# Optimization experiments

Measured on AMD Instinct MI355X. Metric: run time of the kernel, lower is better.

## Reference

```python
import jax, jax.numpy as jnp
import numpy as np

N = 50000   # nodes
E = 800000  # edges
D = 256     # in = hidden = out channels
R = 16      # num_relations (last index reserved for self-loops)
B = 8       # num_bases
LN_EPS = 1e-5


def setup_inputs() -> dict:
    key = jax.random.key(0)
    ks = jax.random.split(key, 20)
    s_basis = np.sqrt(2.0 / (D + D)).astype(np.float32)  # glorot-ish scale
    s_att = np.sqrt(2.0 / (R + B)).astype(np.float32)
    inp = {
        "x": jax.random.normal(ks[0], (N, D), dtype=jnp.float32),
        "edge_index": jax.random.randint(ks[1], (2, E), 0, N),
        "edge_type": jax.random.randint(ks[2], (E,), 0, R),
        "edge_attr": jax.random.uniform(ks[3], (E,), dtype=jnp.float32),
        # layer 1 params
        "basis1": jax.random.normal(ks[4], (B, D, D), dtype=jnp.float32) * s_basis,
        "att1": jax.random.normal(ks[5], (R, B), dtype=jnp.float32) * s_att,
        "root1": jax.random.normal(ks[6], (D, D), dtype=jnp.float32) * s_basis,
        "bias1": jnp.zeros((D,), dtype=jnp.float32),
        "ln1_g": jnp.ones((D,), dtype=jnp.float32),
        "ln1_b": jnp.zeros((D,), dtype=jnp.float32),
        # layer 2 params
        "basis2": jax.random.normal(ks[7], (B, D, D), dtype=jnp.float32) * s_basis,
        "att2": jax.random.normal(ks[8], (R, B), dtype=jnp.float32) * s_att,
        "root2": jax.random.normal(ks[9], (D, D), dtype=jnp.float32) * s_basis,
        "bias2": jnp.zeros((D,), dtype=jnp.float32),
        "ln2_g": jnp.ones((D,), dtype=jnp.float32),
        "ln2_b": jnp.zeros((D,), dtype=jnp.float32),
    }
    return inp


def _layer_norm(x, g, b):
    mu = jnp.mean(x, axis=-1, keepdims=True)
    var = jnp.mean(jnp.square(x - mu), axis=-1, keepdims=True)
    return (x - mu) * jax.lax.rsqrt(var + LN_EPS) * g + b


def _rgcn_layer(x, edge_index, edge_type, edge_attr, basis, att, root, bias):
    n = x.shape[0]
    r = att.shape[0]
    # W_r = sum_b a_rb V_b ; then per-relation transform of every node.
    weight = jnp.einsum('rb,bio->rio', att, basis)          # [R, D, D]
    H = jnp.einsum('ni,rio->nro', x, weight)                # [N, R, D]
    # append self-loops with relation index R-1 and confidence 1.0
    loop = jnp.arange(n, dtype=edge_index.dtype)
    src = jnp.concatenate([edge_index[0], loop])
    dst = jnp.concatenate([edge_index[1], loop])
    et = jnp.concatenate([edge_type, jnp.full((n,), r - 1, dtype=edge_type.dtype)])
    ea = jnp.concatenate([edge_attr, jnp.ones((n,), dtype=x.dtype)])
    msg = H[src, et] * ea[:, None]                          # [E+N, D]
    summ = jax.ops.segment_sum(msg, dst, num_segments=n)
    cnt = jax.ops.segment_sum(jnp.ones_like(ea), dst, num_segments=n)
    agg = summ / cnt[:, None]                               # scatter-mean (cnt >= 1 via self-loops)
    return agg + x @ root + bias


def reference(x, edge_index, edge_type, edge_attr,
              basis1, att1, root1, bias1, ln1_g, ln1_b,
              basis2, att2, root2, bias2, ln2_g, ln2_b):
    # input_proj / output_proj are Identity since in == hidden == out.
    h = x
    h_out = _rgcn_layer(h, edge_index, edge_type, edge_attr, basis1, att1, root1, bias1)
    h = jax.nn.relu(_layer_norm(h + h_out, ln1_g, ln1_b))
    h_out = _rgcn_layer(h, edge_index, edge_type, edge_attr, basis2, att2, root2, bias2)
    h = jax.nn.relu(_layer_norm(h + h_out, ln2_g, ln2_b))
    return h
```

## Files before the change

kernel.cpp:

```cpp
#include <hip/hip_runtime.h>
#include <stdint.h>

#define D 256
#define RREL 16
#define BB 8
#define K9 2304
#define LN_EPS 1e-5f
#define NT (K9 / 64)
#define BUFB 49152

typedef __attribute__((ext_vector_type(8))) short frag8;
typedef __attribute__((ext_vector_type(4))) float floatx4;
typedef __attribute__((ext_vector_type(2))) float float2v;
typedef __attribute__((ext_vector_type(2))) unsigned int uint2v;

__device__ __forceinline__ unsigned short f2bf(float f) {
    union { float f; uint32_t u; } v; v.f = f;
    uint32_t r = (v.u + 0x7FFFu + ((v.u >> 16) & 1u)) >> 16;
    return (unsigned short)r;
}
__device__ __forceinline__ float bf2f(unsigned short u) {
    union { uint32_t u; float f; } v; v.u = (uint32_t)u << 16;
    return v.f;
}
__device__ __forceinline__ float2v bfpair(uint32_t d) {
    union { uint32_t u; float f; } lo, hi;
    lo.u = d << 16; hi.u = d & 0xFFFF0000u;
    return (float2v){lo.f, hi.f};
}

__device__ __forceinline__ float2v pk_mul(float2v a, float2v b) {
    float2v d;
    asm("v_pk_mul_f32 %0, %1, %2" : "=v"(d) : "v"(a), "v"(b));
    return d;
}
__device__ __forceinline__ void pk_fma_lo(float2v& acc, float2v c, float2v x) {
    asm("v_pk_fma_f32 %0, %1, %2, %0 op_sel:[0,0,0] op_sel_hi:[1,0,1]"
        : "+v"(acc) : "v"(c), "v"(x));
}
__device__ __forceinline__ void pk_fma_hi(float2v& acc, float2v c, float2v x) {
    asm("v_pk_fma_f32 %0, %1, %2, %0 op_sel:[0,1,0] op_sel_hi:[1,1,1]"
        : "+v"(acc) : "v"(c), "v"(x));
}

__device__ __forceinline__ void gl2lds16(const unsigned short* g, char* l) {
    __builtin_amdgcn_global_load_lds((const __attribute__((address_space(1))) void*)g,
                                     (__attribute__((address_space(3))) void*)l, 16, 0, 0);
}

__device__ __forceinline__ void nt_store4(unsigned short* p, ushort4 v) {
    uint2v u;
    u.x = (uint32_t)v.x | ((uint32_t)v.y << 16);
    u.y = (uint32_t)v.z | ((uint32_t)v.w << 16);
    __builtin_nontemporal_store(u, (uint2v*)p);
}

__global__ __launch_bounds__(256) void k_cvt(const float* __restrict__ src,
                                             unsigned short* __restrict__ dst, int n4) {
    int i = blockIdx.x * 256 + threadIdx.x;
    if (i >= n4) return;
    float4 v = ((const float4*)src)[i];
    ushort4 o = make_ushort4(f2bf(v.x), f2bf(v.y), f2bf(v.z), f2bf(v.w));
    ((ushort4*)dst)[i] = o;
}

__global__ __launch_bounds__(256) void k_deg(const int* __restrict__ ei,
                                             int* __restrict__ deg, int E) {
    int t = blockIdx.x * 256 + threadIdx.x;
    int stride = gridDim.x * 256;
    int d[8];
#pragma unroll
    for (int j = 0; j < 8; ++j) {
        int e = t + j * stride;
        d[j] = (e < E) ? ei[E + e] : -1;
    }
#pragma unroll
    for (int j = 0; j < 8; ++j)
        if (d[j] >= 0) atomicAdd(&deg[d[j]], 1);
}

__global__ __launch_bounds__(256) void k_scan1(const int* __restrict__ deg,
                                               int* __restrict__ csum, int N) {
    __shared__ int sh[256];
    int n = blockIdx.x * 256 + threadIdx.x;
    sh[threadIdx.x] = (n < N) ? deg[n] : 0;
    __syncthreads();
    for (int off = 128; off > 0; off >>= 1) {
        if (threadIdx.x < off) sh[threadIdx.x] += sh[threadIdx.x + off];
        __syncthreads();
    }
    if (threadIdx.x == 0) csum[blockIdx.x] = sh[0];
}

__global__ __launch_bounds__(256) void k_scan3(const int* __restrict__ deg,
                                               const int* __restrict__ csum, int nch,
                                               int* __restrict__ rowptr,
                                               int* __restrict__ cursor,
                                               float* __restrict__ cnt, int N) {
    __shared__ int sh[256];
    int tid = threadIdx.x;
    int bid = blockIdx.x;
    int base;
    if (nch <= 256) {
        int c = (tid < nch) ? csum[tid] : 0;
        sh[tid] = c;
        __syncthreads();
        for (int off = 1; off < 256; off <<= 1) {
            int t = (tid >= off) ? sh[tid - off] : 0;
            __syncthreads();
            sh[tid] += t;
            __syncthreads();
        }
        base = sh[bid] - csum[bid];
        if (bid == 0 && tid == 255) rowptr[N] = sh[255];
        __syncthreads();
    } else {
        int s = 0;
        for (int i = 0; i < bid; ++i) s += csum[i];
        base = s;
        if (bid == 0 && tid == 0) {
            int tot = 0;
            for (int i = 0; i < nch; ++i) tot += csum[i];
            rowptr[N] = tot;
        }
    }
    int n = bid * 256 + tid;
    int v = (n < N) ? deg[n] : 0;
    sh[tid] = v;
    __syncthreads();
    for (int off = 1; off < 256; off <<= 1) {
        int t = (tid >= off) ? sh[tid - off] : 0;
        __syncthreads();
        sh[tid] += t;
        __syncthreads();
    }
    int excl = sh[tid] - v + base;
    if (n < N) {
        rowptr[n] = excl;
        cursor[n] = excl;
        cnt[n] = (float)(v + 1);
    }
}

__global__ __launch_bounds__(256) void k_scatter(const int* __restrict__ ei,
                                                 const int* __restrict__ et,
                                                 const float* __restrict__ ea,
                                                 int* __restrict__ cursor,
                                                 int2* __restrict__ ep, int E) {
    int t = blockIdx.x * 256 + threadIdx.x;
    int stride = gridDim.x * 256;
    int src[8], dst[8], typ[8]; float w[8]; bool v[8];
#pragma unroll
    for (int j = 0; j < 8; ++j) {
        int e = t + j * stride;
        v[j] = (e < E);
        if (v[j]) { src[j] = ei[e]; dst[j] = ei[E + e]; typ[j] = et[e]; w[j] = ea[e]; }
    }
    int p[8];
#pragma unroll
    for (int j = 0; j < 8; ++j)
        if (v[j]) p[j] = atomicAdd(&cursor[dst[j]], 1);
#pragma unroll
    for (int j = 0; j < 8; ++j)
        if (v[j]) ep[p[j]] = make_int2(src[j] | (typ[j] << 24), __float_as_int(w[j]));
}

__global__ __launch_bounds__(256) void k_prep_w(const float* __restrict__ basis,
                                                const float* __restrict__ root,
                                                unsigned short* __restrict__ Wt) {
    __shared__ float tile[64][65];
    int k0 = blockIdx.x * 64, o0 = blockIdx.y * 64;
    const float* src = (k0 < BB * D) ? (basis + (size_t)k0 * D)
                                     : (root + (size_t)(k0 - BB * D) * D);
    int tid = threadIdx.x;
#pragma unroll
    for (int t = 0; t < 16; ++t) {
        int idx = t * 256 + tid;
        int kk = idx >> 6, oo = idx & 63;
        tile[kk][oo] = src[(size_t)kk * D + o0 + oo];
    }
    __syncthreads();
#pragma unroll
    for (int t = 0; t < 16; ++t) {
        int idx = t * 256 + tid;
        int oo = idx >> 6, kk = idx & 63;
        Wt[(size_t)(o0 + oo) * K9 + k0 + kk] = f2bf(tile[kk][oo]);
    }
}

__device__ __forceinline__ void edge_fma(float2v g2[4][4], float2v c0, float2v c1,
                                         float2v c2, float2v c3,
                                         float2v x0, float2v x1) {
    pk_fma_lo(g2[0][0], c0, x0); pk_fma_lo(g2[1][0], c1, x0);
    pk_fma_lo(g2[2][0], c2, x0); pk_fma_lo(g2[3][0], c3, x0);
    pk_fma_hi(g2[0][1], c0, x0); pk_fma_hi(g2[1][1], c1, x0);
    pk_fma_hi(g2[2][1], c2, x0); pk_fma_hi(g2[3][1], c3, x0);
    pk_fma_lo(g2[0][2], c0, x1); pk_fma_lo(g2[1][2], c1, x1);
    pk_fma_lo(g2[2][2], c2, x1); pk_fma_lo(g2[3][2], c3, x1);
    pk_fma_hi(g2[0][3], c0, x1); pk_fma_hi(g2[1][3], c1, x1);
    pk_fma_hi(g2[3][3], c3, x1); pk_fma_hi(g2[2][3], c2, x1);
}

__device__ __forceinline__ void do_edge(float2v g2[4][4], const float* att_s,
                                        int2 pe, uint2 ud) {
    int r = (unsigned)pe.x >> 24;
    const float4* Ar = (const float4*)&att_s[r * BB];
    float4 a0 = Ar[0], a1 = Ar[1];
    float we = __int_as_float(pe.y);
    float2v w2 = {we, we};
    float2v c0 = pk_mul(w2, (float2v){a0.x, a0.y});
    float2v c1 = pk_mul(w2, (float2v){a0.z, a0.w});
    float2v c2 = pk_mul(w2, (float2v){a1.x, a1.y});
    float2v c3 = pk_mul(w2, (float2v){a1.z, a1.w});
    float2v x0 = bfpair(ud.x), x1 = bfpair(ud.y);
    edge_fma(g2, c0, c1, c2, c3, x0, x1);
}

__global__ __launch_bounds__(256) void k_gather(
    const unsigned short* __restrict__ xb, const float* __restrict__ att,
    const int* __restrict__ rowptr, const int2* __restrict__ ep,
    const float* __restrict__ cnt, unsigned short* __restrict__ G,
    int n0, int rows, int N) {
    __shared__ __align__(32) float att_s[RREL * BB];
    int tid = threadIdx.x;
    if (tid < RREL * BB) att_s[tid] = att[tid];
    __syncthreads();
    int wv = tid >> 6, lane = tid & 63;
    int rloc = blockIdx.x * 4 + wv;
    if (rloc >= rows) return;
    int n = n0 + rloc;
    unsigned short* gout = G + (size_t)rloc * K9 + lane * 4;
    if (n >= N) {
        ushort4 z = make_ushort4(0, 0, 0, 0);
#pragma unroll
        for (int b = 0; b <= BB; ++b) nt_store4(gout + b * D, z);
        return;
    }
    uint2 xu = *(const uint2*)&xb[(size_t)n * D + lane * 4];
    float2v xs0 = bfpair(xu.x), xs1 = bfpair(xu.y);
    float xv[4] = {xs0.x, xs0.y, xs1.x, xs1.y};

    float2v g2[4][4];
#pragma unroll
    for (int bp = 0; bp < 4; ++bp) {
        float2v ap = {att_s[(RREL - 1) * BB + 2 * bp],
                      att_s[(RREL - 1) * BB + 2 * bp + 1]};
#pragma unroll
        for (int j = 0; j < 4; ++j) {
            float2v xs = {xv[j], xv[j]};
            g2[bp][j] = ap * xs;
        }
    }

    int e0 = rowptr[n], e1 = rowptr[n + 1];
    int e = e0;
    for (; e + 4 <= e1; e += 4) {
        int2 pa = ep[e], pb = ep[e + 1], pc = ep[e + 2], pd = ep[e + 3];
        uint2 uA = *(const uint2*)&xb[(size_t)(pa.x & 0xFFFFFF) * D + lane * 4];
        uint2 uB = *(const uint2*)&xb[(size_t)(pb.x & 0xFFFFFF) * D + lane * 4];
        uint2 uC = *(const uint2*)&xb[(size_t)(pc.x & 0xFFFFFF) * D + lane * 4];
        uint2 uD = *(const uint2*)&xb[(size_t)(pd.x & 0xFFFFFF) * D + lane * 4];
        __builtin_amdgcn_sched_barrier(0);
        do_edge(g2, att_s, pa, uA);
        do_edge(g2, att_s, pb, uB);
        do_edge(g2, att_s, pc, uC);
        do_edge(g2, att_s, pd, uD);
    }
    if (e + 2 <= e1) {
        int2 pa = ep[e], pb = ep[e + 1];
        uint2 uA = *(const uint2*)&xb[(size_t)(pa.x & 0xFFFFFF) * D + lane * 4];
        uint2 uB = *(const uint2*)&xb[(size_t)(pb.x & 0xFFFFFF) * D + lane * 4];
        __builtin_amdgcn_sched_barrier(0);
        do_edge(g2, att_s, pa, uA);
        do_edge(g2, att_s, pb, uB);
        e += 2;
    }
    if (e < e1) {
        int2 pa = ep[e];
        uint2 uA = *(const uint2*)&xb[(size_t)(pa.x & 0xFFFFFF) * D + lane * 4];
        do_edge(g2, att_s, pa, uA);
    }
#pragma unroll
    for (int bp = 0; bp < 4; ++bp) {
        ushort4 o0 = make_ushort4(f2bf(g2[bp][0].x), f2bf(g2[bp][1].x),
                                  f2bf(g2[bp][2].x), f2bf(g2[bp][3].x));
        nt_store4(gout + (2 * bp) * D, o0);
        ushort4 o1 = make_ushort4(f2bf(g2[bp][0].y), f2bf(g2[bp][1].y),
                                  f2bf(g2[bp][2].y), f2bf(g2[bp][3].y));
        nt_store4(gout + (2 * bp + 1) * D, o1);
    }
    float cn = cnt[n];
    ushort4 o = make_ushort4(f2bf(cn * xv[0]), f2bf(cn * xv[1]),
                             f2bf(cn * xv[2]), f2bf(cn * xv[3]));
    nt_store4(gout + BB * D, o);
}

__global__ __launch_bounds__(1024, 4) void k_gemm(
    const unsigned short* __restrict__ G, const unsigned short* __restrict__ Wt,
    const float* __restrict__ hin, const float* __restrict__ cnt,
    const float* __restrict__ bias, const float* __restrict__ gln,
    const float* __restrict__ bln, float* __restrict__ hout,
    unsigned short* __restrict__ houtb, int n0, int N) {
    __shared__ __align__(16) char smem[2 * BUFB];
    float* ps   = (float*)smem;
    float* pq   = ps + 512;
    float* mu_s = ps + 1024;
    float* rs_s = ps + 1152;

    int tid = threadIdx.x;
    int wv = tid >> 6, lane = tid & 63;
    int quad = lane >> 4, l16 = lane & 15;
    int wm = wv >> 2, wn = wv & 3;
    int grow = blockIdx.x * 128;
    int nb = n0 + grow;

    int arow_s = tid >> 3, aslot_s = tid & 7;
    const unsigned short* gA =
        G + (size_t)(grow + arow_s) * K9 + ((aslot_s ^ (arow_s & 7)) << 3);
    char* lA = smem + (tid << 4);
    const unsigned short* gB[2]; char* lB[2];
#pragma unroll
    for (int t = 0; t < 2; ++t) {
        int c = t * 1024 + tid;
        int brow = c >> 3, bslot = c & 7;
        gB[t] = Wt + (size_t)brow * K9 + ((bslot ^ (brow & 7)) << 3);
        lB[t] = smem + 16384 + (c << 4);
    }

    floatx4 acc[2][4];
#pragma unroll
    for (int mf = 0; mf < 2; ++mf)
#pragma unroll
        for (int nf = 0; nf < 4; ++nf) acc[mf][nf] = (floatx4){0.f, 0.f, 0.f, 0.f};

    auto STAGE = [&](int it, int soff) {
        int koff = it * 64;
        gl2lds16(gA + koff, lA + soff);
        gl2lds16(gB[0] + koff, lB[0] + soff);
        gl2lds16(gB[1] + koff, lB[1] + soff);
    };
    auto COMPUTE = [&](int soff) {
        const char* Ab = smem + soff;
        const char* Bb = Ab + 16384;
#pragma unroll
        for (int kc = 0; kc < 2; ++kc) {
            int g = kc * 4 + quad;
            frag8 a[2], b[4];
#pragma unroll
            for (int mf = 0; mf < 2; ++mf) {
                int arow = wm * 32 + mf * 16 + l16;
                a[mf] = *(const frag8*)(Ab + arow * 128 + ((g ^ (arow & 7)) << 4));
            }
#pragma unroll
            for (int nf = 0; nf < 4; ++nf) {
                int brow = wn * 64 + nf * 16 + l16;
                b[nf] = *(const frag8*)(Bb + brow * 128 + ((g ^ (brow & 7)) << 4));
            }
#pragma unroll
            for (int mf = 0; mf < 2; ++mf)
#pragma unroll
                for (int nf = 0; nf < 4; ++nf)
                    acc[mf][nf] = __builtin_amdgcn_mfma_f32_16x16x32_bf16(
                        a[mf], b[nf], acc[mf][nf], 0, 0, 0);
        }
    };

    STAGE(0, 0);
    __syncthreads();
    for (int it = 0; it < NT; it += 2) {
        STAGE(it + 1, BUFB);
        COMPUTE(0);
        __syncthreads();
        if (it + 2 < NT) STAGE(it + 2, 0);
        COMPUTE(BUFB);
        __syncthreads();
    }

    int col[4]; float bic[4];
#pragma unroll
    for (int nf = 0; nf < 4; ++nf) {
        col[nf] = wn * 64 + nf * 16 + l16;
        bic[nf] = bias[col[nf]];
    }
#pragma unroll
    for (int mf = 0; mf < 2; ++mf) {
#pragma unroll
        for (int r = 0; r < 4; ++r) {
            int row = wm * 32 + mf * 16 + quad * 4 + r;
            int n = nb + row;
            float s = 0.f, sq = 0.f;
            if (n < N) {
                float inv = 1.0f / cnt[n];
                const float* hp = hin + (size_t)n * D;
#pragma unroll
                for (int nf = 0; nf < 4; ++nf) {
                    float v = acc[mf][nf][r] * inv + hp[col[nf]] + bic[nf];
                    acc[mf][nf][r] = v;
                    s += v; sq += v * v;
                }
            }
            s += __shfl_xor(s, 1); sq += __shfl_xor(sq, 1);
            s += __shfl_xor(s, 2); sq += __shfl_xor(sq, 2);
            s += __shfl_xor(s, 4); sq += __shfl_xor(sq, 4);
            s += __shfl_xor(s, 8); sq += __shfl_xor(sq, 8);
            if (l16 == 0) {
                ps[row * 4 + wn] = s;
                pq[row * 4 + wn] = sq;
            }
        }
    }
    __syncthreads();
    if (tid < 128) {
        float s  = ps[tid * 4] + ps[tid * 4 + 1] + ps[tid * 4 + 2] + ps[tid * 4 + 3];
        float sq = pq[tid * 4] + pq[tid * 4 + 1] + pq[tid * 4 + 2] + pq[tid * 4 + 3];
        float mu = s * (1.f / D);
        mu_s[tid] = mu;
        rs_s[tid] = rsqrtf(sq * (1.f / D) - mu * mu + LN_EPS);
    }
    __syncthreads();

    float gc[4], bc[4];
#pragma unroll
    for (int nf = 0; nf < 4; ++nf) {
        gc[nf] = gln[col[nf]];
        bc[nf] = bln[col[nf]];
    }
#pragma unroll
    for (int mf = 0; mf < 2; ++mf) {
#pragma unroll
        for (int r = 0; r < 4; ++r) {
            int row = wm * 32 + mf * 16 + quad * 4 + r;
            int n = nb + row;
            if (n >= N) continue;
            float mu = mu_s[row], rs = rs_s[row];
            float* op = hout + (size_t)n * D;
#pragma unroll
            for (int nf = 0; nf < 4; ++nf) {
                float o = fmaxf((acc[mf][nf][r] - mu) * rs * gc[nf] + bc[nf], 0.f);
                op[col[nf]] = o;
                if (houtb) houtb[(size_t)n * D + col[nf]] = f2bf(o);
            }
        }
    }
}

extern "C" void kernel_launch(void* const* d_in, const int* in_sizes, int n_in,
                              void* d_out, int out_size, void* d_ws, size_t ws_size,
                              hipStream_t stream) {
    const float* x      = (const float*)d_in[0];
    const int*   ei     = (const int*)d_in[1];
    const int*   et     = (const int*)d_in[2];
    const float* ea     = (const float*)d_in[3];
    const float* basis1 = (const float*)d_in[4];
    const float* att1   = (const float*)d_in[5];
    const float* root1  = (const float*)d_in[6];
    const float* bias1  = (const float*)d_in[7];
    const float* g1     = (const float*)d_in[8];
    const float* b1     = (const float*)d_in[9];
    const float* basis2 = (const float*)d_in[10];
    const float* att2   = (const float*)d_in[11];
    const float* root2  = (const float*)d_in[12];
    const float* bias2  = (const float*)d_in[13];
    const float* g2     = (const float*)d_in[14];
    const float* b2     = (const float*)d_in[15];
    float* out = (float*)d_out;

    int N = in_sizes[0] / D;
    int E = in_sizes[2];
    int nch = (N + 255) / 256;
    int Mp = ((N + 63) / 64) * 64;
    int T = Mp / 64;
    int Tpad = (T + 1) & ~1;

    char* p = (char*)d_ws;
    size_t used = 0;
    auto alloc = [&](size_t bytes) {
        char* q = p;
        size_t a = (bytes + 255) & ~(size_t)255;
        p += a; used += a;
        return q;
    };
    float*          h1     = (float*)alloc((size_t)N * D * 4);
    unsigned short* xb     = (unsigned short*)alloc((size_t)N * D * 2);
    unsigned short* h1b    = (unsigned short*)alloc((size_t)N * D * 2);
    unsigned short* Wt     = (unsigned short*)alloc((size_t)K9 * D * 2);
    int*            deg    = (int*)alloc((size_t)N * 4);
    int*            rowptr = (int*)alloc((size_t)(N + 1) * 4);
    int*            cursor = (int*)alloc((size_t)N * 4);
    float*          cnt    = (float*)alloc((size_t)N * 4);
    int2*           ep     = (int2*)alloc((size_t)E * 8);
    int*            csum   = (int*)alloc((size_t)nch * 4);
    size_t remain = (ws_size > used + 256) ? (ws_size - used - 256) : 0;
    size_t tile_bytes = (size_t)64 * K9 * 2;
    int ct_max = (int)(remain / tile_bytes);
    if (ct_max < 2) ct_max = 2;
    if (ct_max > Tpad) ct_max = Tpad;
    unsigned short* G = (unsigned short*)alloc((size_t)ct_max * tile_bytes);

    int nch2 = (Tpad + ct_max - 1) / ct_max;
    int ct = (Tpad + nch2 - 1) / nch2;
    ct = (ct + 1) & ~1;
    if (ct > ct_max) ct = ct_max & ~1;
    if (ct < 2) ct = 2;

    hipMemsetAsync(deg, 0, (size_t)N * 4, stream);
    int gE8 = (E + 2047) / 2048;
    k_deg<<<gE8, 256, 0, stream>>>(ei, deg, E);
    k_scan1<<<nch, 256, 0, stream>>>(deg, csum, N);
    k_scan3<<<nch, 256, 0, stream>>>(deg, csum, nch, rowptr, cursor, cnt, N);
    k_scatter<<<gE8, 256, 0, stream>>>(ei, et, ea, cursor, ep, E);
    k_cvt<<<(N * D / 4 + 255) / 256, 256, 0, stream>>>(x, xb, N * D / 4);

    const float* bas[2]  = {basis1, basis2};
    const float* attp[2] = {att1, att2};
    const float* rt[2]   = {root1, root2};
    const float* bi[2]   = {bias1, bias2};
    const float* lg[2]   = {g1, g2};
    const float* lb[2]   = {b1, b2};
    const unsigned short* gin[2] = {xb, h1b};
    const float* hres[2] = {x, h1};
    float*          hof[2] = {h1, out};
    unsigned short* hob[2] = {h1b, nullptr};

    for (int L = 0; L < 2; ++L) {
        k_prep_w<<<dim3(K9 / 64, D / 64), 256, 0, stream>>>(bas[L], rt[L], Wt);
        for (int c0 = 0; c0 < Tpad; c0 += ct) {
            int tiles = (Tpad - c0 < ct) ? (Tpad - c0) : ct;
            int rows = tiles * 64;
            int n0 = c0 * 64;
            k_gather<<<rows / 4, 256, 0, stream>>>(gin[L], attp[L], rowptr, ep,
                                                   cnt, G, n0, rows, N);
            k_gemm<<<rows / 128, 1024, 0, stream>>>(G, Wt, hres[L], cnt, bi[L],
                                                    lg[L], lb[L], hof[L], hob[L],
                                                    n0, N);
        }
    }
}
```

Before: 675.4 us.

## Read root-term activations directly in GEMM instead of staging them in G

The gather kernel no longer writes the cnt-scaled self features as a ninth K-slice of the G buffer, so G shrinks from 2304 to 2048 columns. The GEMM streams the last K-chunk straight from the bf16 node features into a separate accumulator that is added without the 1/cnt scaling. This cuts gather write traffic and G read traffic. The G stores also switch from nontemporal to ordinary stores. In exchange the GEMM holds a second accumulator set, which adds register pressure, and padded rows may read past the end of the feature array.

```diff
diff --git a/kernel.cpp b/kernel.cpp
--- a/kernel.cpp
+++ b/kernel.cpp
@@ -5,6 +5,7 @@
 #define RREL 16
 #define BB 8
 #define K9 2304
+#define KG 2048
 #define LN_EPS 1e-5f
 #define NT (K9 / 64)
 #define BUFB 49152
@@ -12,7 +13,6 @@
 typedef __attribute__((ext_vector_type(8))) short frag8;
 typedef __attribute__((ext_vector_type(4))) float floatx4;
 typedef __attribute__((ext_vector_type(2))) float float2v;
-typedef __attribute__((ext_vector_type(2))) unsigned int uint2v;
 
 __device__ __forceinline__ unsigned short f2bf(float f) {
     union { float f; uint32_t u; } v; v.f = f;
@@ -46,13 +46,6 @@
 __device__ __forceinline__ void gl2lds16(const unsigned short* g, char* l) {
     __builtin_amdgcn_global_load_lds((const __attribute__((address_space(1))) void*)g,
                                      (__attribute__((address_space(3))) void*)l, 16, 0, 0);
-}
-
-__device__ __forceinline__ void nt_store4(unsigned short* p, ushort4 v) {
-    uint2v u;
-    u.x = (uint32_t)v.x | ((uint32_t)v.y << 16);
-    u.y = (uint32_t)v.z | ((uint32_t)v.w << 16);
-    __builtin_nontemporal_store(u, (uint2v*)p);
 }
 
 __global__ __launch_bounds__(256) void k_cvt(const float* __restrict__ src,
@@ -198,7 +191,7 @@
     pk_fma_lo(g2[0][2], c0, x1); pk_fma_lo(g2[1][2], c1, x1);
     pk_fma_lo(g2[2][2], c2, x1); pk_fma_lo(g2[3][2], c3, x1);
     pk_fma_hi(g2[0][3], c0, x1); pk_fma_hi(g2[1][3], c1, x1);
-    pk_fma_hi(g2[3][3], c3, x1); pk_fma_hi(g2[2][3], c2, x1);
+    pk_fma_hi(g2[2][3], c2, x1); pk_fma_hi(g2[3][3], c3, x1);
 }
 
 __device__ __forceinline__ void do_edge(float2v g2[4][4], const float* att_s,
@@ -219,8 +212,7 @@
 __global__ __launch_bounds__(256) void k_gather(
     const unsigned short* __restrict__ xb, const float* __restrict__ att,
     const int* __restrict__ rowptr, const int2* __restrict__ ep,
-    const float* __restrict__ cnt, unsigned short* __restrict__ G,
-    int n0, int rows, int N) {
+    unsigned short* __restrict__ G, int n0, int rows, int N) {
     __shared__ __align__(32) float att_s[RREL * BB];
     int tid = threadIdx.x;
     if (tid < RREL * BB) att_s[tid] = att[tid];
@@ -229,11 +221,11 @@
     int rloc = blockIdx.x * 4 + wv;
     if (rloc >= rows) return;
     int n = n0 + rloc;
-    unsigned short* gout = G + (size_t)rloc * K9 + lane * 4;
+    unsigned short* gout = G + (size_t)rloc * KG + lane * 4;
     if (n >= N) {
         ushort4 z = make_ushort4(0, 0, 0, 0);
 #pragma unroll
-        for (int b = 0; b <= BB; ++b) nt_store4(gout + b * D, z);
+        for (int b = 0; b < BB; ++b) *(ushort4*)(gout + b * D) = z;
         return;
     }
     uint2 xu = *(const uint2*)&xb[(size_t)n * D + lane * 4];
@@ -284,19 +276,16 @@
     for (int bp = 0; bp < 4; ++bp) {
         ushort4 o0 = make_ushort4(f2bf(g2[bp][0].x), f2bf(g2[bp][1].x),
                                   f2bf(g2[bp][2].x), f2bf(g2[bp][3].x));
-        nt_store4(gout + (2 * bp) * D, o0);
+        *(ushort4*)(gout + (2 * bp) * D) = o0;
         ushort4 o1 = make_ushort4(f2bf(g2[bp][0].y), f2bf(g2[bp][1].y),
                                   f2bf(g2[bp][2].y), f2bf(g2[bp][3].y));
-        nt_store4(gout + (2 * bp + 1) * D, o1);
-    }
-    float cn = cnt[n];
-    ushort4 o = make_ushort4(f2bf(cn * xv[0]), f2bf(cn * xv[1]),
-                             f2bf(cn * xv[2]), f2bf(cn * xv[3]));
-    nt_store4(gout + BB * D, o);
+        *(ushort4*)(gout + (2 * bp + 1) * D) = o1;
+    }
 }
 
 __global__ __launch_bounds__(1024, 4) void k_gemm(
-    const unsigned short* __restrict__ G, const unsigned short* __restrict__ Wt,
+    const unsigned short* __restrict__ G, const unsigned short* __restrict__ xb,
+    const unsigned short* __restrict__ Wt,
     const float* __restrict__ hin, const float* __restrict__ cnt,
     const float* __restrict__ bias, const float* __restrict__ gln,
     const float* __restrict__ bln, float* __restrict__ hout,
@@ -315,8 +304,9 @@
     int nb = n0 + grow;
 
     int arow_s = tid >> 3, aslot_s = tid & 7;
-    const unsigned short* gA =
-        G + (size_t)(grow + arow_s) * K9 + ((aslot_s ^ (arow_s & 7)) << 3);
+    int swzA = (aslot_s ^ (arow_s & 7)) << 3;
+    const unsigned short* gAG = G + (size_t)(grow + arow_s) * KG + swzA;
+    const unsigned short* gAX = xb + (size_t)(nb + arow_s) * D + swzA;
     char* lA = smem + (tid << 4);
     const unsigned short* gB[2]; char* lB[2];
 #pragma unroll
@@ -328,18 +318,24 @@
     }
 
     floatx4 acc[2][4];
+    floatx4 acc2[2][4];
 #pragma unroll
     for (int mf = 0; mf < 2; ++mf)
 #pragma unroll
-        for (int nf = 0; nf < 4; ++nf) acc[mf][nf] = (floatx4){0.f, 0.f, 0.f, 0.f};
+        for (int nf = 0; nf < 4; ++nf) {
+            acc[mf][nf]  = (floatx4){0.f, 0.f, 0.f, 0.f};
+            acc2[mf][nf] = (floatx4){0.f, 0.f, 0.f, 0.f};
+        }
 
     auto STAGE = [&](int it, int soff) {
+        const unsigned short* sa =
+            (it < 32) ? (gAG + it * 64) : (gAX + (it - 32) * 64);
+        gl2lds16(sa, lA + soff);
         int koff = it * 64;
-        gl2lds16(gA + koff, lA + soff);
         gl2lds16(gB[0] + koff, lB[0] + soff);
         gl2lds16(gB[1] + koff, lB[1] + soff);
     };
-    auto COMPUTE = [&](int soff) {
+    auto COMPUTE = [&](int soff, floatx4 (&ac)[2][4]) {
         const char* Ab = smem + soff;
         const char* Bb = Ab + 16384;
 #pragma unroll
@@ -360,19 +356,27 @@
             for (int mf = 0; mf < 2; ++mf)
 #pragma unroll
                 for (int nf = 0; nf < 4; ++nf)
-                    acc[mf][nf] = __builtin_amdgcn_mfma_f32_16x16x32_bf16(
-                        a[mf], b[nf], acc[mf][nf], 0, 0, 0);
+                    ac[mf][nf] = __builtin_amdgcn_mfma_f32_16x16x32_bf16(
+                        a[mf], b[nf], ac[mf][nf], 0, 0, 0);
         }
     };
 
     STAGE(0, 0);
     __syncthreads();
-    for (int it = 0; it < NT; it += 2) {
+    for (int it = 0; it < 32; it += 2) {
         STAGE(it + 1, BUFB);
-        COMPUTE(0);
+        COMPUTE(0, acc);
+        __syncthreads();
+        STAGE(it + 2, 0);
+        COMPUTE(BUFB, acc);
+        __syncthreads();
+    }
+    for (int it = 32; it < NT; it += 2) {
+        STAGE(it + 1, BUFB);
+        COMPUTE(0, acc2);
         __syncthreads();
         if (it + 2 < NT) STAGE(it + 2, 0);
-        COMPUTE(BUFB);
+        COMPUTE(BUFB, acc2);
         __syncthreads();
     }
 
@@ -394,7 +398,8 @@
                 const float* hp = hin + (size_t)n * D;
 #pragma unroll
                 for (int nf = 0; nf < 4; ++nf) {
-                    float v = acc[mf][nf][r] * inv + hp[col[nf]] + bic[nf];
+                    float v = acc[mf][nf][r] * inv + acc2[mf][nf][r]
+                            + hp[col[nf]] + bic[nf];
                     acc[mf][nf][r] = v;
                     s += v; sq += v * v;
                 }
@@ -491,7 +496,7 @@
     int2*           ep     = (int2*)alloc((size_t)E * 8);
     int*            csum   = (int*)alloc((size_t)nch * 4);
     size_t remain = (ws_size > used + 256) ? (ws_size - used - 256) : 0;
-    size_t tile_bytes = (size_t)64 * K9 * 2;
+    size_t tile_bytes = (size_t)64 * KG * 2;
     int ct_max = (int)(remain / tile_bytes);
     if (ct_max < 2) ct_max = 2;
     if (ct_max > Tpad) ct_max = Tpad;
@@ -529,10 +534,10 @@
             int rows = tiles * 64;
             int n0 = c0 * 64;
             k_gather<<<rows / 4, 256, 0, stream>>>(gin[L], attp[L], rowptr, ep,
-                                                   cnt, G, n0, rows, N);
-            k_gemm<<<rows / 128, 1024, 0, stream>>>(G, Wt, hres[L], cnt, bi[L],
-                                                    lg[L], lb[L], hof[L], hob[L],
-                                                    n0, N);
-        }
-    }
-}
+                                                   G, n0, rows, N);
+            k_gemm<<<rows / 128, 1024, 0, stream>>>(G, gin[L], Wt, hres[L], cnt,
+                                                    bi[L], lg[L], lb[L], hof[L],
+                                                    hob[L], n0, N);
+        }
+    }
+}
```

After: 618.0 us. -8.5%, faster.
